# Performance work log

Hardware: AMD Instinct MI355X
Metric: run time of the kernel (lower is better)

The kernel has to match this reference:

```python
import jax, jax.numpy as jnp
import numpy as np

D_MODEL = 1024
NUM_HEADS = 16
D_K = D_MODEL // NUM_HEADS
SCALE = float(np.sqrt(D_K))


def setup_inputs() -> dict:
    key = jax.random.key(0)
    ks = jax.random.split(key, 11)
    B, S = 4, 2048
    std = 1.0 / np.sqrt(D_MODEL)
    return {
        "query": jax.random.normal(ks[0], (B, S, D_MODEL), jnp.float32),
        "key": jax.random.normal(ks[1], (B, S, D_MODEL), jnp.float32),
        "value": jax.random.normal(ks[2], (B, S, D_MODEL), jnp.float32),
        "w_q": jax.random.normal(ks[3], (D_MODEL, D_MODEL), jnp.float32) * std,
        "b_q": jnp.zeros((D_MODEL,), jnp.float32),
        "w_k": jax.random.normal(ks[4], (D_MODEL, D_MODEL), jnp.float32) * std,
        "b_k": jnp.zeros((D_MODEL,), jnp.float32),
        "w_v": jax.random.normal(ks[5], (D_MODEL, D_MODEL), jnp.float32) * std,
        "b_v": jnp.zeros((D_MODEL,), jnp.float32),
        "w_o": jax.random.normal(ks[6], (D_MODEL, D_MODEL), jnp.float32) * std,
        "b_o": jnp.zeros((D_MODEL,), jnp.float32),
    }


def reference(query, key, value, w_q, b_q, w_k, b_k, w_v, b_v, w_o, b_o):
    B, S, _ = query.shape
    # torch Linear: x @ W.T + b
    def proj(x, w, b):
        y = x @ w.T + b                      # [B,S,D]
        return y.reshape(B, -1, NUM_HEADS, D_K).transpose(0, 2, 1, 3)  # [B,H,S,dk]

    Q = proj(query, w_q, b_q)
    K = proj(key, w_k, b_k)
    V = proj(value, w_v, b_v)

    scores = jnp.einsum("bhqd,bhkd->bhqk", Q, K) / SCALE   # [B,H,S,S]
    attn = jax.nn.softmax(scores, axis=-1)                  # dropout = identity (eval)
    ctx = jnp.einsum("bhqk,bhkd->bhqd", attn, V)            # [B,H,S,dk]
    ctx = ctx.transpose(0, 2, 1, 3).reshape(B, -1, D_MODEL) # [B,S,D]
    out = ctx @ w_o.T + b_o
    return out, attn
```

## Files before the change

kernel.cpp:

```cpp
#include <hip/hip_runtime.h>

typedef __bf16 bf16;
typedef __bf16 bf16x8 __attribute__((ext_vector_type(8)));
typedef __bf16 bf16x4 __attribute__((ext_vector_type(4)));
typedef float f32x4 __attribute__((ext_vector_type(4)));

#define B_SZ   4
#define S_LEN  2048
#define DM     1024
#define NH     16
#define DKH    64
#define MROWS  (B_SZ * S_LEN)

#if __has_builtin(__builtin_amdgcn_exp2f)
#define EXP2(x) __builtin_amdgcn_exp2f(x)
#else
#define EXP2(x) exp2f(x)
#endif

__device__ __forceinline__ int swz_(int row) { return ((row ^ (row >> 3)) & 7) << 4; }

__device__ __forceinline__ void gload_lds16(const void* g, void* l) {
  __builtin_amdgcn_global_load_lds(
      (const __attribute__((address_space(1))) void*)g,
      (__attribute__((address_space(3))) void*)l, 16, 0, 0);
}

__global__ __launch_bounds__(256) void cvt_f32_bf16(const float* __restrict__ in,
                                                    bf16* __restrict__ out, int n8) {
  for (int i = blockIdx.x * blockDim.x + threadIdx.x; i < n8; i += gridDim.x * blockDim.x) {
    const float4* p = (const float4*)(in + (size_t)i * 8);
    float4 a = p[0], b = p[1];
    bf16x8 o;
    o[0] = (bf16)a.x; o[1] = (bf16)a.y; o[2] = (bf16)a.z; o[3] = (bf16)a.w;
    o[4] = (bf16)b.x; o[5] = (bf16)b.y; o[6] = (bf16)b.z; o[7] = (bf16)b.w;
    *(bf16x8*)(out + (size_t)i * 8) = o;
  }
}

__global__ __launch_bounds__(256) void transpose_v(const bf16* __restrict__ V,
                                                   bf16* __restrict__ VT) {
  __shared__ bf16 T[64 * 64];
  const int tid = threadIdx.x;
  const int bh = blockIdx.x >> 5;
  const int s0 = (blockIdx.x & 31) * 64;
  const bf16* src = V + ((size_t)bh * S_LEN + s0) * DKH;
  bf16x8 vv[2];
#pragma unroll
  for (int r = 0; r < 2; ++r) {
    int c = r * 256 + tid;
    vv[r] = *(const bf16x8*)(src + (c >> 3) * DKH + (c & 7) * 8);
  }
#pragma unroll
  for (int r = 0; r < 2; ++r) {
    int c = r * 256 + tid;
    int s = c >> 3, d0 = (c & 7) * 8;
#pragma unroll
    for (int j = 0; j < 8; ++j) {
      int row = d0 + j;
      *(bf16*)((char*)T + row * 128 + ((s * 2) ^ swz_(row))) = vv[r][j];
    }
  }
  __syncthreads();
#pragma unroll
  for (int r = 0; r < 2; ++r) {
    int c = r * 256 + tid;
    int d = c >> 3, off = (c & 7) * 16;
    bf16x8 o = *(const bf16x8*)((const char*)T + d * 128 + (off ^ swz_(d)));
    *(bf16x8*)(VT + ((size_t)bh * DKH + d) * S_LEN + s0 + (c & 7) * 8) = o;
  }
}

template <int MODE>
__global__ __launch_bounds__(256) void gemm_bt(const bf16* __restrict__ A,
                                               const bf16* __restrict__ Bm,
                                               const float* __restrict__ bias,
                                               void* __restrict__ out) {
  constexpr int BM = 128, BN = 128, BK = 64, K = DM, N = DM;
  __shared__ bf16 As[BM * BK];
  __shared__ bf16 Bs[BN * BK];
  const int tid = threadIdx.x;
  const int l = tid & 63;
  const int w = tid >> 6;
  const int wr = w >> 1, wc = w & 1;
  const int m0 = (blockIdx.x >> 3) * BM;
  const int n0 = (blockIdx.x & 7) * BN;
  const int lrow = l & 15;
  const int lk = (l >> 4) * 8;

  f32x4 acc[4][4] = {};

  for (int kt = 0; kt < K; kt += BK) {
    __syncthreads();
#pragma unroll
    for (int r = 0; r < 4; ++r) {
      int c = r * 256 + tid;
      int row = c >> 3;
      int cb = ((c & 7) * 16) ^ swz_(row);
      gload_lds16((const char*)(A + (size_t)(m0 + row) * K + kt) + cb, (char*)As + c * 16);
      gload_lds16((const char*)(Bm + (size_t)(n0 + row) * K + kt) + cb, (char*)Bs + c * 16);
    }
    __syncthreads();
#pragma unroll
    for (int kk = 0; kk < BK; kk += 32) {
      bf16x8 a[4], b[4];
#pragma unroll
      for (int i = 0; i < 4; ++i) {
        int ar = wr * 64 + i * 16 + lrow;
        int br = wc * 64 + i * 16 + lrow;
        a[i] = *(const bf16x8*)((const char*)As + ar * 128 + (((kk + lk) * 2) ^ swz_(ar)));
        b[i] = *(const bf16x8*)((const char*)Bs + br * 128 + (((kk + lk) * 2) ^ swz_(br)));
      }
#pragma unroll
      for (int i = 0; i < 4; ++i)
#pragma unroll
        for (int j = 0; j < 4; ++j)
          acc[i][j] = __builtin_amdgcn_mfma_f32_16x16x32_bf16(a[i], b[j], acc[i][j], 0, 0, 0);
    }
  }

#pragma unroll
  for (int i = 0; i < 4; ++i) {
#pragma unroll
    for (int j = 0; j < 4; ++j) {
#pragma unroll
      for (int r = 0; r < 4; ++r) {
        int row = m0 + wr * 64 + i * 16 + (l >> 4) * 4 + r;
        int col = n0 + wc * 64 + j * 16 + (l & 15);
        float v = acc[i][j][r] + bias[col];
        if (MODE == 0) {
          int bb = row >> 11, ss = row & 2047, hh = col >> 6, dd = col & 63;
          ((bf16*)out)[(((size_t)bb * NH + hh) * S_LEN + ss) * DKH + dd] = (bf16)v;
        } else {
          ((float*)out)[(size_t)row * N + col] = v;
        }
      }
    }
  }
}

__global__ __launch_bounds__(256, 3) void attn_fused(const bf16* __restrict__ Q,
                                                     const bf16* __restrict__ Kg,
                                                     const bf16* __restrict__ VT,
                                                     float* __restrict__ attn,
                                                     bf16* __restrict__ ctx) {
  constexpr int QT = 128, KT = 64, PSP = 72, NT = S_LEN / KT;
  __shared__ bf16 Ks[KT * DKH];
  __shared__ bf16 Vts[DKH * KT];
  __shared__ bf16 Ps[QT * PSP];

  const int tid = threadIdx.x, l = tid & 63, w = tid >> 6;
  const int bh = blockIdx.x >> 4;
  const int q0 = (blockIdx.x & 15) * QT;
  const bf16* Qb = Q + (size_t)bh * S_LEN * DKH;
  const bf16* Kb = Kg + (size_t)bh * S_LEN * DKH;
  const bf16* VTb = VT + (size_t)bh * DKH * S_LEN;
  const int lrow = l & 15, lk = (l >> 4) * 8;
  const int g4 = (l >> 4) * 4;
  const float c2 = 0.18033688011f;

  bf16x8 qf[2][2];
#pragma unroll
  for (int m = 0; m < 2; ++m)
#pragma unroll
    for (int h = 0; h < 2; ++h)
      qf[m][h] = *(const bf16x8*)(Qb + (size_t)(q0 + w * 32 + m * 16 + lrow) * DKH + h * 32 + lk);

  auto stageK = [&](int kt) {
#pragma unroll
    for (int r = 0; r < 2; ++r) {
      int c = r * 256 + tid;
      int row = c >> 3;
      int cb = ((c & 7) * 16) ^ swz_(row);
      gload_lds16((const char*)(Kb + (size_t)(kt + row) * DKH) + cb, (char*)Ks + c * 16);
    }
  };
  auto stageV = [&](int kt) {
#pragma unroll
    for (int r = 0; r < 2; ++r) {
      int c = r * 256 + tid;
      int row = c >> 3;
      int cb = ((c & 7) * 16) ^ swz_(row);
      gload_lds16((const char*)(VTb + (size_t)row * S_LEN + kt) + cb, (char*)Vts + c * 16);
    }
  };

  float lsum[2] = {0.f, 0.f};
  for (int t = 0; t < NT; ++t) {
    __syncthreads();
    stageK(t * KT);
    __syncthreads();
    f32x4 st[2][4] = {};
#pragma unroll
    for (int h = 0; h < 2; ++h)
#pragma unroll
      for (int n = 0; n < 4; ++n) {
        int kr = n * 16 + lrow;
        bf16x8 b = *(const bf16x8*)((const char*)Ks + kr * 128 + (((h * 32 + lk) * 2) ^ swz_(kr)));
        st[0][n] = __builtin_amdgcn_mfma_f32_16x16x32_bf16(b, qf[0][h], st[0][n], 0, 0, 0);
        st[1][n] = __builtin_amdgcn_mfma_f32_16x16x32_bf16(b, qf[1][h], st[1][n], 0, 0, 0);
      }
#pragma unroll
    for (int m = 0; m < 2; ++m)
#pragma unroll
      for (int n = 0; n < 4; ++n)
#pragma unroll
        for (int r = 0; r < 4; ++r)
          lsum[m] += EXP2(st[m][n][r] * c2);
  }

  float invl[2];
#pragma unroll
  for (int m = 0; m < 2; ++m) {
    float ll = lsum[m];
    ll += __shfl_xor(ll, 16);
    ll += __shfl_xor(ll, 32);
    invl[m] = 1.0f / ll;
  }

  f32x4 oc[2][4] = {};
  for (int t = 0; t < NT; ++t) {
    const int kt = t * KT;
    __syncthreads();
    stageK(kt);
    stageV(kt);
    __syncthreads();
    f32x4 st[2][4] = {};
#pragma unroll
    for (int h = 0; h < 2; ++h)
#pragma unroll
      for (int n = 0; n < 4; ++n) {
        int kr = n * 16 + lrow;
        bf16x8 b = *(const bf16x8*)((const char*)Ks + kr * 128 + (((h * 32 + lk) * 2) ^ swz_(kr)));
        st[0][n] = __builtin_amdgcn_mfma_f32_16x16x32_bf16(b, qf[0][h], st[0][n], 0, 0, 0);
        st[1][n] = __builtin_amdgcn_mfma_f32_16x16x32_bf16(b, qf[1][h], st[1][n], 0, 0, 0);
      }
#pragma unroll
    for (int m = 0; m < 2; ++m) {
      const int qr = w * 32 + m * 16 + lrow;
      float* arow = attn + (size_t)bh * S_LEN * S_LEN + (size_t)(q0 + qr) * S_LEN + kt + g4;
#pragma unroll
      for (int n = 0; n < 4; ++n) {
        f32x4 p4;
#pragma unroll
        for (int r = 0; r < 4; ++r) p4[r] = EXP2(st[m][n][r] * c2) * invl[m];
        *(f32x4*)(arow + n * 16) = p4;
        bf16x4 pk;
#pragma unroll
        for (int r = 0; r < 4; ++r) pk[r] = (bf16)p4[r];
        *(bf16x4*)((char*)Ps + qr * (PSP * 2) + n * 32 + g4 * 2) = pk;
      }
    }
#pragma unroll
    for (int kk = 0; kk < KT; kk += 32) {
      bf16x8 bfr[4];
#pragma unroll
      for (int n = 0; n < 4; ++n) {
        int vr = n * 16 + lrow;
        bfr[n] = *(const bf16x8*)((const char*)Vts + vr * 128 + (((kk + lk) * 2) ^ swz_(vr)));
      }
#pragma unroll
      for (int m = 0; m < 2; ++m) {
        bf16x8 pa = *(const bf16x8*)(Ps + (w * 32 + m * 16 + lrow) * PSP + kk + lk);
#pragma unroll
        for (int n = 0; n < 4; ++n)
          oc[m][n] = __builtin_amdgcn_mfma_f32_16x16x32_bf16(pa, bfr[n], oc[m][n], 0, 0, 0);
      }
    }
  }

  const int bb = bh >> 4, hh = bh & 15;
#pragma unroll
  for (int m = 0; m < 2; ++m)
#pragma unroll
    for (int n = 0; n < 4; ++n)
#pragma unroll
      for (int r = 0; r < 4; ++r) {
        int row = q0 + w * 32 + m * 16 + (l >> 4) * 4 + r;
        int col = hh * DKH + n * 16 + (l & 15);
        ctx[((size_t)bb * S_LEN + row) * DM + col] = (bf16)oc[m][n][r];
      }
}

extern "C" void kernel_launch(void* const* d_in, const int* in_sizes, int n_in,
                              void* d_out, int out_size, void* d_ws, size_t ws_size,
                              hipStream_t stream) {
  const float* query = (const float*)d_in[0];
  const float* key_i = (const float*)d_in[1];
  const float* value = (const float*)d_in[2];
  const float* w_q = (const float*)d_in[3];
  const float* b_q = (const float*)d_in[4];
  const float* w_k = (const float*)d_in[5];
  const float* b_k = (const float*)d_in[6];
  const float* w_v = (const float*)d_in[7];
  const float* b_v = (const float*)d_in[8];
  const float* w_o = (const float*)d_in[9];
  const float* b_o = (const float*)d_in[10];

  char* ws = (char*)d_ws;
  bf16* Xb = (bf16*)(ws);
  bf16* Wb = (bf16*)(ws + ((size_t)16 << 20));
  bf16* Qb = (bf16*)(ws + ((size_t)18 << 20));
  bf16* Kb = (bf16*)(ws + ((size_t)34 << 20));
  bf16* Vb = (bf16*)(ws + ((size_t)50 << 20));
  bf16* Cb = (bf16*)(ws + ((size_t)66 << 20));

  float* outp = (float*)d_out;
  float* attnp = outp + (size_t)B_SZ * S_LEN * DM;

  const int NX = MROWS * DM / 8;
  const int NW = DM * DM / 8;
  dim3 blk(256);

  cvt_f32_bf16<<<2048, blk, 0, stream>>>(query, Xb, NX);
  cvt_f32_bf16<<<512, blk, 0, stream>>>(w_q, Wb, NW);
  gemm_bt<0><<<512, blk, 0, stream>>>(Xb, Wb, b_q, Qb);
  cvt_f32_bf16<<<2048, blk, 0, stream>>>(key_i, Xb, NX);
  cvt_f32_bf16<<<512, blk, 0, stream>>>(w_k, Wb, NW);
  gemm_bt<0><<<512, blk, 0, stream>>>(Xb, Wb, b_k, Kb);
  cvt_f32_bf16<<<2048, blk, 0, stream>>>(value, Xb, NX);
  cvt_f32_bf16<<<512, blk, 0, stream>>>(w_v, Wb, NW);
  gemm_bt<0><<<512, blk, 0, stream>>>(Xb, Wb, b_v, Vb);

  transpose_v<<<B_SZ * NH * (S_LEN / 64), blk, 0, stream>>>(Vb, Xb);
  cvt_f32_bf16<<<512, blk, 0, stream>>>(w_o, Wb, NW);

  attn_fused<<<B_SZ * NH * (S_LEN / 128), blk, 0, stream>>>(Qb, Kb, Xb, attnp, Cb);

  gemm_bt<1><<<512, blk, 0, stream>>>(Cb, Wb, b_o, (void*)outp);
}
```

Measured before the change: 549.5 us.

## Double-buffer K/V LDS tiles to overlap staging with MFMA compute

```diff
diff --git a/kernel.cpp b/kernel.cpp
--- a/kernel.cpp
+++ b/kernel.cpp
@@ -145,8 +145,8 @@
                                                      float* __restrict__ attn,
                                                      bf16* __restrict__ ctx) {
   constexpr int QT = 128, KT = 64, PSP = 72, NT = S_LEN / KT;
-  __shared__ bf16 Ks[KT * DKH];
-  __shared__ bf16 Vts[DKH * KT];
+  __shared__ bf16 Ks[2][KT * DKH];
+  __shared__ bf16 Vts[2][DKH * KT];
   __shared__ bf16 Ps[QT * PSP];
 
   const int tid = threadIdx.x, l = tid & 63, w = tid >> 6;
@@ -166,37 +166,38 @@
     for (int h = 0; h < 2; ++h)
       qf[m][h] = *(const bf16x8*)(Qb + (size_t)(q0 + w * 32 + m * 16 + lrow) * DKH + h * 32 + lk);
 
-  auto stageK = [&](int kt) {
+  auto stageK = [&](int kt, int buf) {
 #pragma unroll
     for (int r = 0; r < 2; ++r) {
       int c = r * 256 + tid;
       int row = c >> 3;
       int cb = ((c & 7) * 16) ^ swz_(row);
-      gload_lds16((const char*)(Kb + (size_t)(kt + row) * DKH) + cb, (char*)Ks + c * 16);
+      gload_lds16((const char*)(Kb + (size_t)(kt + row) * DKH) + cb, (char*)Ks[buf] + c * 16);
     }
   };
-  auto stageV = [&](int kt) {
+  auto stageV = [&](int kt, int buf) {
 #pragma unroll
     for (int r = 0; r < 2; ++r) {
       int c = r * 256 + tid;
       int row = c >> 3;
       int cb = ((c & 7) * 16) ^ swz_(row);
-      gload_lds16((const char*)(VTb + (size_t)row * S_LEN + kt) + cb, (char*)Vts + c * 16);
+      gload_lds16((const char*)(VTb + (size_t)row * S_LEN + kt) + cb, (char*)Vts[buf] + c * 16);
     }
   };
 
+  stageK(0, 0);
   float lsum[2] = {0.f, 0.f};
   for (int t = 0; t < NT; ++t) {
+    const int p = t & 1;
     __syncthreads();
-    stageK(t * KT);
-    __syncthreads();
+    stageK(((t + 1) & (NT - 1)) * KT, p ^ 1);
     f32x4 st[2][4] = {};
 #pragma unroll
     for (int h = 0; h < 2; ++h)
 #pragma unroll
       for (int n = 0; n < 4; ++n) {
         int kr = n * 16 + lrow;
-        bf16x8 b = *(const bf16x8*)((const char*)Ks + kr * 128 + (((h * 32 + lk) * 2) ^ swz_(kr)));
+        bf16x8 b = *(const bf16x8*)((const char*)Ks[p] + kr * 128 + (((h * 32 + lk) * 2) ^ swz_(kr)));
         st[0][n] = __builtin_amdgcn_mfma_f32_16x16x32_bf16(b, qf[0][h], st[0][n], 0, 0, 0);
         st[1][n] = __builtin_amdgcn_mfma_f32_16x16x32_bf16(b, qf[1][h], st[1][n], 0, 0, 0);
       }
@@ -218,20 +219,22 @@
     invl[m] = 1.0f / ll;
   }
 
+  stageV(0, 0);
   f32x4 oc[2][4] = {};
   for (int t = 0; t < NT; ++t) {
+    const int p = t & 1;
     const int kt = t * KT;
+    const int ktn = ((t + 1) & (NT - 1)) * KT;
     __syncthreads();
-    stageK(kt);
-    stageV(kt);
-    __syncthreads();
+    stageK(ktn, p ^ 1);
+    stageV(ktn, p ^ 1);
     f32x4 st[2][4] = {};
 #pragma unroll
     for (int h = 0; h < 2; ++h)
 #pragma unroll
       for (int n = 0; n < 4; ++n) {
         int kr = n * 16 + lrow;
-        bf16x8 b = *(const bf16x8*)((const char*)Ks + kr * 128 + (((h * 32 + lk) * 2) ^ swz_(kr)));
+        bf16x8 b = *(const bf16x8*)((const char*)Ks[p] + kr * 128 + (((h * 32 + lk) * 2) ^ swz_(kr)));
         st[0][n] = __builtin_amdgcn_mfma_f32_16x16x32_bf16(b, qf[0][h], st[0][n], 0, 0, 0);
         st[1][n] = __builtin_amdgcn_mfma_f32_16x16x32_bf16(b, qf[1][h], st[1][n], 0, 0, 0);
       }
@@ -257,7 +260,7 @@
 #pragma unroll
       for (int n = 0; n < 4; ++n) {
         int vr = n * 16 + lrow;
-        bfr[n] = *(const bf16x8*)((const char*)Vts + vr * 128 + (((kk + lk) * 2) ^ swz_(vr)));
+        bfr[n] = *(const bf16x8*)((const char*)Vts[p] + vr * 128 + (((kk + lk) * 2) ^ swz_(vr)));
       }
 #pragma unroll
       for (int m = 0; m < 2; ++m) {
```

Result: no change. 558.5 us (+1.6%).

## Load K and V fragments directly from global memory instead of LDS staging

Applied to the files above, without the earlier changes.

```diff
diff --git a/kernel.cpp b/kernel.cpp
--- a/kernel.cpp
+++ b/kernel.cpp
@@ -145,8 +145,6 @@
                                                      float* __restrict__ attn,
                                                      bf16* __restrict__ ctx) {
   constexpr int QT = 128, KT = 64, PSP = 72, NT = S_LEN / KT;
-  __shared__ bf16 Ks[KT * DKH];
-  __shared__ bf16 Vts[DKH * KT];
   __shared__ bf16 Ps[QT * PSP];
 
   const int tid = threadIdx.x, l = tid & 63, w = tid >> 6;
@@ -166,39 +164,18 @@
     for (int h = 0; h < 2; ++h)
       qf[m][h] = *(const bf16x8*)(Qb + (size_t)(q0 + w * 32 + m * 16 + lrow) * DKH + h * 32 + lk);
 
-  auto stageK = [&](int kt) {
-#pragma unroll
-    for (int r = 0; r < 2; ++r) {
-      int c = r * 256 + tid;
-      int row = c >> 3;
-      int cb = ((c & 7) * 16) ^ swz_(row);
-      gload_lds16((const char*)(Kb + (size_t)(kt + row) * DKH) + cb, (char*)Ks + c * 16);
-    }
-  };
-  auto stageV = [&](int kt) {
-#pragma unroll
-    for (int r = 0; r < 2; ++r) {
-      int c = r * 256 + tid;
-      int row = c >> 3;
-      int cb = ((c & 7) * 16) ^ swz_(row);
-      gload_lds16((const char*)(VTb + (size_t)row * S_LEN + kt) + cb, (char*)Vts + c * 16);
-    }
-  };
-
   float lsum[2] = {0.f, 0.f};
+#pragma unroll 2
   for (int t = 0; t < NT; ++t) {
-    __syncthreads();
-    stageK(t * KT);
-    __syncthreads();
+    const bf16* Kt = Kb + (size_t)t * KT * DKH;
     f32x4 st[2][4] = {};
 #pragma unroll
     for (int h = 0; h < 2; ++h)
 #pragma unroll
       for (int n = 0; n < 4; ++n) {
-        int kr = n * 16 + lrow;
-        bf16x8 b = *(const bf16x8*)((const char*)Ks + kr * 128 + (((h * 32 + lk) * 2) ^ swz_(kr)));
-        st[0][n] = __builtin_amdgcn_mfma_f32_16x16x32_bf16(b, qf[0][h], st[0][n], 0, 0, 0);
-        st[1][n] = __builtin_amdgcn_mfma_f32_16x16x32_bf16(b, qf[1][h], st[1][n], 0, 0, 0);
+        bf16x8 kf = *(const bf16x8*)(Kt + (n * 16 + lrow) * DKH + h * 32 + lk);
+        st[0][n] = __builtin_amdgcn_mfma_f32_16x16x32_bf16(kf, qf[0][h], st[0][n], 0, 0, 0);
+        st[1][n] = __builtin_amdgcn_mfma_f32_16x16x32_bf16(kf, qf[1][h], st[1][n], 0, 0, 0);
       }
 #pragma unroll
     for (int m = 0; m < 2; ++m)
@@ -221,20 +198,22 @@
   f32x4 oc[2][4] = {};
   for (int t = 0; t < NT; ++t) {
     const int kt = t * KT;
-    __syncthreads();
-    stageK(kt);
-    stageV(kt);
-    __syncthreads();
+    const bf16* Kt = Kb + (size_t)kt * DKH;
     f32x4 st[2][4] = {};
 #pragma unroll
     for (int h = 0; h < 2; ++h)
 #pragma unroll
       for (int n = 0; n < 4; ++n) {
-        int kr = n * 16 + lrow;
-        bf16x8 b = *(const bf16x8*)((const char*)Ks + kr * 128 + (((h * 32 + lk) * 2) ^ swz_(kr)));
-        st[0][n] = __builtin_amdgcn_mfma_f32_16x16x32_bf16(b, qf[0][h], st[0][n], 0, 0, 0);
-        st[1][n] = __builtin_amdgcn_mfma_f32_16x16x32_bf16(b, qf[1][h], st[1][n], 0, 0, 0);
-      }
+        bf16x8 kf = *(const bf16x8*)(Kt + (n * 16 + lrow) * DKH + h * 32 + lk);
+        st[0][n] = __builtin_amdgcn_mfma_f32_16x16x32_bf16(kf, qf[0][h], st[0][n], 0, 0, 0);
+        st[1][n] = __builtin_amdgcn_mfma_f32_16x16x32_bf16(kf, qf[1][h], st[1][n], 0, 0, 0);
+      }
+    bf16x8 vf[2][4];
+#pragma unroll
+    for (int kg = 0; kg < 2; ++kg)
+#pragma unroll
+      for (int n = 0; n < 4; ++n)
+        vf[kg][n] = *(const bf16x8*)(VTb + (size_t)(n * 16 + lrow) * S_LEN + kt + kg * 32 + lk);
 #pragma unroll
     for (int m = 0; m < 2; ++m) {
       const int qr = w * 32 + m * 16 + lrow;
@@ -252,21 +231,14 @@
       }
     }
 #pragma unroll
-    for (int kk = 0; kk < KT; kk += 32) {
-      bf16x8 bfr[4];
-#pragma unroll
-      for (int n = 0; n < 4; ++n) {
-        int vr = n * 16 + lrow;
-        bfr[n] = *(const bf16x8*)((const char*)Vts + vr * 128 + (((kk + lk) * 2) ^ swz_(vr)));
-      }
+    for (int kg = 0; kg < 2; ++kg)
 #pragma unroll
       for (int m = 0; m < 2; ++m) {
-        bf16x8 pa = *(const bf16x8*)(Ps + (w * 32 + m * 16 + lrow) * PSP + kk + lk);
+        bf16x8 pa = *(const bf16x8*)(Ps + (w * 32 + m * 16 + lrow) * PSP + kg * 32 + lk);
 #pragma unroll
         for (int n = 0; n < 4; ++n)
-          oc[m][n] = __builtin_amdgcn_mfma_f32_16x16x32_bf16(pa, bfr[n], oc[m][n], 0, 0, 0);
-      }
-    }
+          oc[m][n] = __builtin_amdgcn_mfma_f32_16x16x32_bf16(pa, vf[kg][n], oc[m][n], 0, 0, 0);
+      }
   }
 
   const int bb = bh >> 4, hh = bh & 15;
```

Measured after the change: 722.3 us. +31.4%, slower.
